# Kernel tuning notes

Hardware: AMD Instinct MI355X
Metric: run time of the kernel (lower is better)

## Reference

```python
import jax, jax.numpy as jnp
import numpy as np

N_ATOMS = 16384
APC = 64            # atoms per conformer
N_CONF = 256        # 64 mols * 4 confs
N_MOL = 64
DEG = 32
E = N_ATOMS * DEG
H = 128             # hidden_channels = num_filters = out_channels
G = 50              # num_gaussians
L = 6               # num_interactions
CUTOFF = 10.0
LOG2 = float(np.log(2.0))


def ssp(x):
    # ShiftedSoftplus: softplus(x) - log(2)
    return jax.nn.softplus(x) - LOG2


def setup_inputs() -> dict:
    key = jax.random.key(0)
    ks = jax.random.split(key, 24)
    rng = np.random.default_rng(0)

    z = jnp.asarray(rng.integers(1, 100, size=(N_ATOMS,)), dtype=jnp.int64 if jax.config.jax_enable_x64 else jnp.int32)
    # positions uniform in a 5A box -> all intra-conformer distances < cutoff
    pos = jax.random.uniform(ks[0], (N_ATOMS, 3), dtype=jnp.float32) * 5.0

    # within-conformer random edges, no self loops (radius_graph surrogate)
    i = np.repeat(np.arange(N_ATOMS), DEG)
    off = rng.integers(1, APC, size=E)
    j = (i // APC) * APC + (i % APC + off) % APC
    edge_index = jnp.asarray(np.stack([j, i]), dtype=jnp.int32)  # [2,E] (source, target)

    atom_to_conf = jnp.asarray(np.arange(N_ATOMS) // APC, dtype=jnp.int32)
    conf_to_mol = jnp.asarray(np.arange(N_CONF) // (N_CONF // N_MOL), dtype=jnp.int32)

    s = 0.05
    p = {
        'emb':     jax.random.normal(ks[1], (120, H), jnp.float32) * s,
        # per-interaction stacked params [L, ...]
        'mlp_w1':  jax.random.normal(ks[2], (L, G, H), jnp.float32) * s,
        'mlp_b1':  jnp.zeros((L, H), jnp.float32),
        'mlp_w2':  jax.random.normal(ks[3], (L, H, H), jnp.float32) * s,
        'mlp_b2':  jnp.zeros((L, H), jnp.float32),
        'cf_w1':   jax.random.normal(ks[4], (L, H, H), jnp.float32) * s,
        'cf_w2':   jax.random.normal(ks[5], (L, H, H), jnp.float32) * s,
        'cf_b2':   jnp.zeros((L, H), jnp.float32),
        'int_w':   jax.random.normal(ks[6], (L, H, H), jnp.float32) * s,
        'int_b':   jnp.zeros((L, H), jnp.float32),
        # readout head
        'out_w1':  jax.random.normal(ks[7], (H, H), jnp.float32) * s,
        'out_b1':  jnp.zeros((H,), jnp.float32),
        'out_w2':  jax.random.normal(ks[8], (H, H), jnp.float32) * s,
        'out_b2':  jnp.zeros((H,), jnp.float32),
        'head_w1': jax.random.normal(ks[9], (H, H // 2), jnp.float32) * s,
        'head_b1': jnp.zeros((H // 2,), jnp.float32),
        'head_w2': jax.random.normal(ks[10], (H // 2, 1), jnp.float32) * s,
        'head_b2': jnp.zeros((1,), jnp.float32),
    }
    return dict(z=z, pos=pos, edge_index=edge_index, atom_to_conf=atom_to_conf,
                conf_to_mol=conf_to_mol, **p)


def reference(z, pos, edge_index, atom_to_conf, conf_to_mol, emb,
              mlp_w1, mlp_b1, mlp_w2, mlp_b2, cf_w1, cf_w2, cf_b2,
              int_w, int_b, out_w1, out_b1, out_w2, out_b2,
              head_w1, head_b1, head_w2, head_b2):
    row, col = edge_index[0], edge_index[1]  # message from row, aggregated at col

    h = emb[z]                                             # [N,H]
    edge_weight = jnp.linalg.norm(pos[row] - pos[col], axis=-1)  # [E]

    # GaussianSmearing
    offset = jnp.linspace(0.0, CUTOFF, G)
    coeff = -0.5 / (offset[1] - offset[0]) ** 2
    edge_attr = jnp.exp(coeff * (edge_weight[:, None] - offset[None, :]) ** 2)  # [E,G]

    C = 0.5 * (jnp.cos(edge_weight * jnp.pi / CUTOFF) + 1.0)  # cosine cutoff [E]

    for l in range(L):
        # filter network on edge features, modulated by cutoff envelope
        Wf = ssp(edge_attr @ mlp_w1[l] + mlp_b1[l]) @ mlp_w2[l] + mlp_b2[l]
        Wf = Wf * C[:, None]                               # [E,H]
        xf = h @ cf_w1[l]                                  # lin1 (no bias) [N,H]
        msg = xf[row] * Wf                                 # gather * filter [E,H]
        agg = jax.ops.segment_sum(msg, col, num_segments=N_ATOMS)  # scatter-add [N,H]
        xc = agg @ cf_w2[l] + cf_b2[l]                     # lin2
        h = h + (ssp(xc) @ int_w[l] + int_b[l])            # act, lin, residual

    h = ssp(h @ out_w1 + out_b1)
    h = h @ out_w2 + out_b2                                # [N,H]

    conf_emb = jax.ops.segment_sum(h, atom_to_conf, num_segments=N_CONF)   # [C,H]
    mol_emb = jax.ops.segment_sum(conf_emb, conf_to_mol, num_segments=N_MOL)  # [M,H]

    out = (ssp(mol_emb @ head_w1 + head_b1) @ head_w2 + head_b2)[:, 0]  # [M]
    return out
```

## Files before the change

### kernel.cpp

```cpp
#include <hip/hip_runtime.h>
#include <math.h>

#define N_ATOMS 16384
#define APC 64
#define N_CONF 256
#define N_MOL 64
#define DEG 32
#define NEDGE (N_ATOMS * DEG)
#define H 128
#define G 50
#define NL 6
#define TP0 512
#define TPB 4096
#define CUTOFF 10.0f

typedef __attribute__((ext_vector_type(8))) short short8_t;
typedef __attribute__((ext_vector_type(4))) float f32x4;

__device__ __forceinline__ float ssp_f(float x) {
  float e = __expf(-fabsf(x));
  return fmaxf(x, 0.f) + __logf(1.f + e) - 0.69314718055994531f;
}
__device__ __forceinline__ unsigned short bf16_rne(float x) {
  unsigned u = __float_as_uint(x);
  unsigned r = u + 0x7FFF + ((u >> 16) & 1);
  return (unsigned short)(r >> 16);
}
__device__ __forceinline__ float bf16_to_f(unsigned short s) {
  return __uint_as_float(((unsigned)s) << 16);
}
__device__ __forceinline__ float bflo(unsigned u) { return __uint_as_float(u << 16); }
__device__ __forceinline__ float bfhi(unsigned u) { return __uint_as_float(u & 0xFFFF0000u); }

__global__ __launch_bounds__(256) void k_setup(
    const float* __restrict__ cf_w1, const float* __restrict__ cf_w2,
    const float* __restrict__ int_w, const float* __restrict__ out_w1,
    const float* __restrict__ out_w2, short* __restrict__ PW,
    const float* __restrict__ w1, const float* __restrict__ b1,
    const float* __restrict__ w2, const float* __restrict__ b2,
    float* __restrict__ T) {
  __shared__ float g2[2][64];
  __shared__ float S2[2][128];
  const int b = blockIdx.x;
  const int tid = threadIdx.x;
  if (b < 160) {
    int e = b * 256 + tid;
    int g = e >> 11, t = e & 2047;
    int kb = t >> 9, rem = t & 511, nt = rem >> 6, lane = rem & 63;
    int quad = lane >> 4, ln = lane & 15;
    int kbase = kb * 32 + quad * 8;
    int n = nt * 16 + ln;
    const float* src;
    if (g < 12) {
      int l = g >> 1;
      src = (g & 1) ? (int_w + l * 16384) : (cf_w2 + l * 16384);
    } else if (g < 18) {
      src = cf_w1 + (g - 12) * 16384;
    } else {
      src = (g == 18) ? out_w1 : out_w2;
    }
    short hv[8], lv[8];
    #pragma unroll
    for (int j = 0; j < 8; j++) {
      float x = src[(kbase + j) * H + n];
      unsigned short hb = bf16_rne(x);
      hv[j] = (short)hb;
      lv[j] = (short)bf16_rne(x - bf16_to_f(hb));
    }
    size_t base = (size_t)g * 32768 + (size_t)t * 8;
    *(short8_t*)&PW[base] = *(short8_t*)hv;
    *(short8_t*)&PW[base + 16384] = *(short8_t*)lv;
  } else {
    int bb = b - 160;
    const int l = bb >> 8;
    const int grp = tid >> 7;
    const int c = tid & 127;
    const int p = (bb & 255) * 2 + grp;
    const float d = (float)p * (CUTOFF / (float)(TP0 - 1));
    const float gspace = CUTOFF / (float)(G - 1);
    const float coeff = -0.5f / (gspace * gspace);
    if (c < G) {
      float x = d - (float)c * gspace;
      g2[grp][c] = __expf(coeff * x * x);
    }
    __syncthreads();
    const float* W1 = w1 + l * G * H;
    float s = b1[l * H + c];
    #pragma unroll 5
    for (int i = 0; i < G; i++) s += g2[grp][i] * W1[i * H + c];
    S2[grp][c] = ssp_f(s);
    __syncthreads();
    const float* W2 = w2 + l * H * H;
    float o = b2[l * H + c];
    #pragma unroll 8
    for (int j = 0; j < H; j++) o += S2[grp][j] * W2[j * H + c];
    float Cc = 0.5f * (__cosf(d * (3.14159265358979f / CUTOFF)) + 1.f);
    T[((size_t)l * TP0 + p) * H + c] = o * Cc;
  }
}

__global__ __launch_bounds__(256) void k_up(const float* __restrict__ T,
                                            unsigned short* __restrict__ Tb) {
  int t = blockIdx.x * 256 + threadIdx.x;
  int l = t >> 17;
  int rem = t & 131071;
  int p4 = rem >> 5, cg = rem & 31;
  int c = cg * 4;
  float u = (float)p4 * ((float)(TP0 - 1) / (float)(TPB - 1));
  int i = (int)u;
  if (i > TP0 - 2) i = TP0 - 2;
  float f = u - (float)i;
  const float* a = T + ((size_t)l * TP0 + i) * H + c;
  float4 v0 = *(const float4*)a;
  float4 v1 = *(const float4*)(a + H);
  ushort4 o;
  o.x = bf16_rne(v0.x + f * (v1.x - v0.x));
  o.y = bf16_rne(v0.y + f * (v1.y - v0.y));
  o.z = bf16_rne(v0.z + f * (v1.z - v0.z));
  o.w = bf16_rne(v0.w + f * (v1.w - v0.w));
  *(ushort4*)&Tb[((size_t)l * TPB + p4) * H + c] = o;
}

#define MFMA(a, b, c) __builtin_amdgcn_mfma_f32_16x16x32_bf16((a), (b), (c), 0, 0, 0)

__device__ __forceinline__ void load_afrags(const short (*AH)[136], const short (*AL)[136],
                                            int rt, int ln, int quad,
                                            short8_t ah[4], short8_t al[4]) {
  #pragma unroll
  for (int kb = 0; kb < 4; kb++) {
    int ko = kb * 32 + quad * 8;
    ah[kb] = *(const short8_t*)&AH[rt * 16 + ln][ko];
    al[kb] = *(const short8_t*)&AL[rt * 16 + ln][ko];
  }
}

__device__ __forceinline__ void gemm2w(const short8_t ah[4], const short8_t al[4],
                                       const short* __restrict__ pw, int nt0, int lane,
                                       f32x4 acc[2]) {
  #pragma unroll
  for (int ct = 0; ct < 2; ct++) {
    int nt = nt0 + ct;
    f32x4 a = {0.f, 0.f, 0.f, 0.f};
    #pragma unroll
    for (int kb = 0; kb < 4; kb++) {
      const short* pb = pw + ((size_t)(kb * 8 + nt) * 64 + lane) * 8;
      short8_t bh = *(const short8_t*)pb;
      short8_t bl = *(const short8_t*)(pb + 16384);
      a = MFMA(ah[kb], bh, a);
      a = MFMA(ah[kb], bl, a);
      a = MFMA(al[kb], bh, a);
    }
    acc[ct] = a;
  }
}

__global__ __launch_bounds__(1024, 1) void k_mega(
    const int* __restrict__ z, const float* __restrict__ pos,
    const int* __restrict__ esrc, const float* __restrict__ emb,
    const unsigned short* __restrict__ Tb, const short* __restrict__ PW,
    const float* __restrict__ cf_b2, const float* __restrict__ int_b,
    const float* __restrict__ out_b1, const float* __restrict__ out_b2,
    float* __restrict__ ce, const float* __restrict__ hw1,
    const float* __restrict__ hb1, const float* __restrict__ hw2,
    const float* __restrict__ hb2, int* __restrict__ cnt,
    float* __restrict__ outp) {
  __shared__ float xs[64][132];
  __shared__ __align__(16) short hH[64][136], hL[64][136];
  __shared__ __align__(16) short S1H[64][136], S1L[64][136];
  __shared__ int pks[2048];
  __shared__ float ps[4][128];
  __shared__ float posL[192];
  __shared__ int is_last;
  const int conf = blockIdx.x;
  const int tid = threadIdx.x;
  const int lane = tid & 63, w = tid >> 6;
  const int quad = lane >> 4, ln = lane & 15;
  const int rt = w & 3, nt0 = (w >> 2) * 2;
  const int eg = lane >> 4, ch0 = (lane & 15) * 8;

  if (tid < 192) posL[tid] = pos[conf * 192 + tid];
  __syncthreads();
  #pragma unroll
  for (int k = 0; k < 2; k++) {
    int e2 = k * 1024 + tid;
    int r = esrc[conf * 2048 + e2];
    int rl = r & (APC - 1);
    int ca = e2 >> 5;
    float dx = posL[rl * 3 + 0] - posL[ca * 3 + 0];
    float dy = posL[rl * 3 + 1] - posL[ca * 3 + 1];
    float dz = posL[rl * 3 + 2] - posL[ca * 3 + 2];
    float d = sqrtf(dx * dx + dy * dy + dz * dz);
    int i = (int)(d * ((float)(TPB - 1) / CUTOFF) + 0.5f);
    if (i > TPB - 1) i = TPB - 1;
    if (i < 0) i = 0;
    pks[e2] = i | (rl << 16);
  }
  {
    int r = tid >> 4, cb = (tid & 15) * 8;
    const float* src = emb + (size_t)z[conf * 64 + r] * H + cb;
    float4 v0 = *(const float4*)src, v1 = *(const float4*)(src + 4);
    float vv[8] = {v0.x, v0.y, v0.z, v0.w, v1.x, v1.y, v1.z, v1.w};
    short hv[8], lv[8];
    #pragma unroll
    for (int u = 0; u < 8; u++) {
      unsigned short hb = bf16_rne(vv[u]);
      hv[u] = (short)hb;
      lv[u] = (short)bf16_rne(vv[u] - bf16_to_f(hb));
    }
    *(short8_t*)&hH[r][cb] = *(short8_t*)hv;
    *(short8_t*)&hL[r][cb] = *(short8_t*)lv;
  }
  __syncthreads();

  {
    short8_t ah[4], al_[4];
    load_afrags(hH, hL, rt, ln, quad, ah, al_);
    f32x4 acc[2];
    gemm2w(ah, al_, PW + (size_t)12 * 32768, nt0, lane, acc);
    #pragma unroll
    for (int ct = 0; ct < 2; ct++)
      #pragma unroll
      for (int reg = 0; reg < 4; reg++)
        xs[rt * 16 + quad * 4 + reg][(nt0 + ct) * 16 + ln] = acc[ct][reg];
  }
  __syncthreads();

  for (int l = 0; l < NL; l++) {
    const unsigned short* Tl = Tb + (size_t)l * TPB * H;
    #pragma unroll 1
    for (int aa = 0; aa < 4; aa++) {
      int a2 = w * 4 + aa;
      int ms[8];
      uint4 tvv[8];
      #pragma unroll
      for (int it = 0; it < 8; it++) ms[it] = pks[a2 * DEG + it * 4 + eg];
      #pragma unroll
      for (int it = 0; it < 8; it++)
        tvv[it] = *(const uint4*)&Tl[(size_t)(ms[it] & 0xFFFF) * H + ch0];
      float acc[8] = {};
      #pragma unroll
      for (int it = 0; it < 8; it++) {
        int sl = ms[it] >> 16;
        const float* xr = &xs[sl][ch0];
        float4 x0 = *(const float4*)xr;
        float4 x1 = *(const float4*)(xr + 4);
        uint4 tv = tvv[it];
        acc[0] += bflo(tv.x) * x0.x; acc[1] += bfhi(tv.x) * x0.y;
        acc[2] += bflo(tv.y) * x0.z; acc[3] += bfhi(tv.y) * x0.w;
        acc[4] += bflo(tv.z) * x1.x; acc[5] += bfhi(tv.z) * x1.y;
        acc[6] += bflo(tv.w) * x1.z; acc[7] += bfhi(tv.w) * x1.w;
      }
      #pragma unroll
      for (int j = 0; j < 8; j++) {
        acc[j] += __shfl_xor(acc[j], 16);
        acc[j] += __shfl_xor(acc[j], 32);
      }
      if (eg == 0) {
        short hv[8], lv[8];
        #pragma unroll
        for (int j = 0; j < 8; j++) {
          unsigned short hb = bf16_rne(acc[j]);
          hv[j] = (short)hb;
          lv[j] = (short)bf16_rne(acc[j] - bf16_to_f(hb));
        }
        *(short8_t*)&S1H[a2][ch0] = *(short8_t*)hv;
        *(short8_t*)&S1L[a2][ch0] = *(short8_t*)lv;
      }
    }
    __syncthreads();
    {
      short8_t ah[4], al_[4];
      load_afrags(S1H, S1L, rt, ln, quad, ah, al_);
      f32x4 acc[2];
      gemm2w(ah, al_, PW + (size_t)(2 * l) * 32768, nt0, lane, acc);
      __syncthreads();
      #pragma unroll
      for (int ct = 0; ct < 2; ct++) {
        int col = (nt0 + ct) * 16 + ln;
        float bb = cf_b2[l * H + col];
        #pragma unroll
        for (int reg = 0; reg < 4; reg++) {
          int row = rt * 16 + quad * 4 + reg;
          float v = ssp_f(acc[ct][reg] + bb);
          unsigned short hb = bf16_rne(v);
          S1H[row][col] = (short)hb;
          S1L[row][col] = (short)bf16_rne(v - bf16_to_f(hb));
        }
      }
    }
    __syncthreads();
    {
      short8_t ah[4], al_[4];
      load_afrags(S1H, S1L, rt, ln, quad, ah, al_);
      f32x4 acc[2];
      gemm2w(ah, al_, PW + (size_t)(2 * l + 1) * 32768, nt0, lane, acc);
      #pragma unroll
      for (int ct = 0; ct < 2; ct++) {
        int col = (nt0 + ct) * 16 + ln;
        float bb = int_b[l * H + col];
        #pragma unroll
        for (int reg = 0; reg < 4; reg++) {
          int row = rt * 16 + quad * 4 + reg;
          float hv = bf16_to_f((unsigned short)hH[row][col]) +
                     bf16_to_f((unsigned short)hL[row][col]);
          float v = acc[ct][reg] + bb + hv;
          unsigned short hb = bf16_rne(v);
          hH[row][col] = (short)hb;
          hL[row][col] = (short)bf16_rne(v - bf16_to_f(hb));
        }
      }
    }
    __syncthreads();
    if (l < NL - 1) {
      short8_t ah[4], al_[4];
      load_afrags(hH, hL, rt, ln, quad, ah, al_);
      f32x4 acc[2];
      gemm2w(ah, al_, PW + (size_t)(13 + l) * 32768, nt0, lane, acc);
      #pragma unroll
      for (int ct = 0; ct < 2; ct++)
        #pragma unroll
        for (int reg = 0; reg < 4; reg++)
          xs[rt * 16 + quad * 4 + reg][(nt0 + ct) * 16 + ln] = acc[ct][reg];
      __syncthreads();
    }
  }

  {
    short8_t ah[4], al_[4];
    load_afrags(hH, hL, rt, ln, quad, ah, al_);
    f32x4 acc[2];
    gemm2w(ah, al_, PW + (size_t)18 * 32768, nt0, lane, acc);
    __syncthreads();
    #pragma unroll
    for (int ct = 0; ct < 2; ct++) {
      int col = (nt0 + ct) * 16 + ln;
      float bb = out_b1[col];
      #pragma unroll
      for (int reg = 0; reg < 4; reg++) {
        int row = rt * 16 + quad * 4 + reg;
        float v = ssp_f(acc[ct][reg] + bb);
        unsigned short hb = bf16_rne(v);
        S1H[row][col] = (short)hb;
        S1L[row][col] = (short)bf16_rne(v - bf16_to_f(hb));
      }
    }
  }
  __syncthreads();
  {
    short8_t ah[4], al_[4];
    load_afrags(S1H, S1L, rt, ln, quad, ah, al_);
    f32x4 acc[2];
    gemm2w(ah, al_, PW + (size_t)19 * 32768, nt0, lane, acc);
    #pragma unroll
    for (int ct = 0; ct < 2; ct++) {
      int col = (nt0 + ct) * 16 + ln;
      float s = acc[ct][0] + acc[ct][1] + acc[ct][2] + acc[ct][3];
      s += __shfl_xor(s, 16);
      s += __shfl_xor(s, 32);
      if (quad == 0) ps[rt][col] = s;
    }
  }
  __syncthreads();
  if (tid < 128) {
    float v = ps[0][tid] + ps[1][tid] + ps[2][tid] + ps[3][tid] + 64.f * out_b2[tid];
    __hip_atomic_store(&ce[conf * 128 + tid], v, __ATOMIC_RELAXED,
                       __HIP_MEMORY_SCOPE_AGENT);
  }
  __syncthreads();
  if (tid == 0) {
    __threadfence();
    int old = __hip_atomic_fetch_add(cnt, 1, __ATOMIC_ACQ_REL,
                                     __HIP_MEMORY_SCOPE_AGENT);
    is_last = (old == N_CONF - 1) ? 1 : 0;
  }
  __syncthreads();
  if (is_last) {
    __threadfence();
    float* mol = &xs[0][0];
    for (int t = tid; t < N_MOL * 128; t += 1024) {
      int m = t >> 7, c = t & 127;
      const float* bb = ce + (size_t)(m * 4) * 128;
      float s = __hip_atomic_load(&bb[c], __ATOMIC_RELAXED, __HIP_MEMORY_SCOPE_AGENT) +
                __hip_atomic_load(&bb[128 + c], __ATOMIC_RELAXED, __HIP_MEMORY_SCOPE_AGENT) +
                __hip_atomic_load(&bb[256 + c], __ATOMIC_RELAXED, __HIP_MEMORY_SCOPE_AGENT) +
                __hip_atomic_load(&bb[384 + c], __ATOMIC_RELAXED, __HIP_MEMORY_SCOPE_AGENT);
      mol[t] = s;
    }
    __syncthreads();
    float* q = (float*)&S1H[0][0];
    for (int t = tid; t < N_MOL * 64; t += 1024) {
      int m = t >> 6, j = t & 63;
      float qq = hb1[j];
      #pragma unroll 8
      for (int c = 0; c < H; c++) qq += mol[m * 128 + c] * hw1[c * 64 + j];
      q[t] = ssp_f(qq);
    }
    __syncthreads();
    if (tid < N_MOL) {
      float o = hb2[0];
      #pragma unroll 8
      for (int j = 0; j < 64; j++) o += q[tid * 64 + j] * hw2[j];
      outp[tid] = o;
    }
  }
}

extern "C" void kernel_launch(void* const* d_in, const int* in_sizes, int n_in,
                              void* d_out, int out_size, void* d_ws, size_t ws_size,
                              hipStream_t stream) {
  const int*   z       = (const int*)d_in[0];
  const float* pos     = (const float*)d_in[1];
  const int*   eidx    = (const int*)d_in[2];
  const float* emb     = (const float*)d_in[5];
  const float* mlp_w1  = (const float*)d_in[6];
  const float* mlp_b1  = (const float*)d_in[7];
  const float* mlp_w2  = (const float*)d_in[8];
  const float* mlp_b2  = (const float*)d_in[9];
  const float* cf_w1   = (const float*)d_in[10];
  const float* cf_w2   = (const float*)d_in[11];
  const float* cf_b2   = (const float*)d_in[12];
  const float* int_w   = (const float*)d_in[13];
  const float* int_b   = (const float*)d_in[14];
  const float* out_w1  = (const float*)d_in[15];
  const float* out_b1  = (const float*)d_in[16];
  const float* out_w2  = (const float*)d_in[17];
  const float* out_b2  = (const float*)d_in[18];
  const float* head_w1 = (const float*)d_in[19];
  const float* head_b1 = (const float*)d_in[20];
  const float* head_w2 = (const float*)d_in[21];
  const float* head_b2 = (const float*)d_in[22];

  char* ws = (char*)d_ws;
  float*          T   = (float*)ws;
  unsigned short* Tb  = (unsigned short*)(ws + 1572864);
  short*          PW  = (short*)(ws + 1572864 + 6291456);
  float*          ce  = (float*)(ws + 9175040);
  int*            cnt = (int*)(ws + 9306112);

  hipMemsetAsync(cnt, 0, 4, stream);
  k_setup<<<1696, 256, 0, stream>>>(cf_w1, cf_w2, int_w, out_w1, out_w2, PW,
                                    mlp_w1, mlp_b1, mlp_w2, mlp_b2, T);
  k_up<<<(NL * TPB * H / 4) / 256, 256, 0, stream>>>(T, Tb);
  k_mega<<<N_CONF, 1024, 0, stream>>>(z, pos, eidx, emb, Tb, PW, cf_b2, int_b,
                                      out_b1, out_b2, ce,
                                      head_w1, head_b1, head_w2, head_b2,
                                      cnt, (float*)d_out);
}
```

Baseline: 260.2 us.

## Fuse table upsampling into mega kernel with grid barrier; retile GEMM waves

Removes the separate k_up launch by having every block of k_mega upsample its slice of the bf16 filter table, then wait on a global atomic-counter barrier before the interaction layers read it. The GEMM wave mapping also changes: each wave now computes two 16-row tiles for one 16-column tile, reusing each B fragment across two MFMAs instead of reusing A fragments across two column tiles. The grid barrier relies on all 256 blocks being co-resident, which holds only if the GPU has at least 256 CUs at one block per CU. It also adds spin-wait latency.

```diff
diff --git a/kernel.cpp b/kernel.cpp
--- a/kernel.cpp
+++ b/kernel.cpp
@@ -99,65 +99,35 @@
   }
 }
 
-__global__ __launch_bounds__(256) void k_up(const float* __restrict__ T,
-                                            unsigned short* __restrict__ Tb) {
-  int t = blockIdx.x * 256 + threadIdx.x;
-  int l = t >> 17;
-  int rem = t & 131071;
-  int p4 = rem >> 5, cg = rem & 31;
-  int c = cg * 4;
-  float u = (float)p4 * ((float)(TP0 - 1) / (float)(TPB - 1));
-  int i = (int)u;
-  if (i > TP0 - 2) i = TP0 - 2;
-  float f = u - (float)i;
-  const float* a = T + ((size_t)l * TP0 + i) * H + c;
-  float4 v0 = *(const float4*)a;
-  float4 v1 = *(const float4*)(a + H);
-  ushort4 o;
-  o.x = bf16_rne(v0.x + f * (v1.x - v0.x));
-  o.y = bf16_rne(v0.y + f * (v1.y - v0.y));
-  o.z = bf16_rne(v0.z + f * (v1.z - v0.z));
-  o.w = bf16_rne(v0.w + f * (v1.w - v0.w));
-  *(ushort4*)&Tb[((size_t)l * TPB + p4) * H + c] = o;
-}
-
 #define MFMA(a, b, c) __builtin_amdgcn_mfma_f32_16x16x32_bf16((a), (b), (c), 0, 0, 0)
 
-__device__ __forceinline__ void load_afrags(const short (*AH)[136], const short (*AL)[136],
-                                            int rt, int ln, int quad,
-                                            short8_t ah[4], short8_t al[4]) {
+__device__ __forceinline__ void gemm_rt2(const short (*AH)[136], const short (*AL)[136],
+                                         const short* __restrict__ pw,
+                                         int rt2, int nt, int lane, int quad, int ln,
+                                         f32x4 acc[2]) {
   #pragma unroll
   for (int kb = 0; kb < 4; kb++) {
+    const short* pb = pw + ((size_t)(kb * 8 + nt) * 64 + lane) * 8;
+    short8_t bh = *(const short8_t*)pb;
+    short8_t bl = *(const short8_t*)(pb + 16384);
     int ko = kb * 32 + quad * 8;
-    ah[kb] = *(const short8_t*)&AH[rt * 16 + ln][ko];
-    al[kb] = *(const short8_t*)&AL[rt * 16 + ln][ko];
-  }
-}
-
-__device__ __forceinline__ void gemm2w(const short8_t ah[4], const short8_t al[4],
-                                       const short* __restrict__ pw, int nt0, int lane,
-                                       f32x4 acc[2]) {
-  #pragma unroll
-  for (int ct = 0; ct < 2; ct++) {
-    int nt = nt0 + ct;
-    f32x4 a = {0.f, 0.f, 0.f, 0.f};
-    #pragma unroll
-    for (int kb = 0; kb < 4; kb++) {
-      const short* pb = pw + ((size_t)(kb * 8 + nt) * 64 + lane) * 8;
-      short8_t bh = *(const short8_t*)pb;
-      short8_t bl = *(const short8_t*)(pb + 16384);
-      a = MFMA(ah[kb], bh, a);
-      a = MFMA(ah[kb], bl, a);
-      a = MFMA(al[kb], bh, a);
-    }
-    acc[ct] = a;
+    #pragma unroll
+    for (int rtt = 0; rtt < 2; rtt++) {
+      int row = rt2 * 32 + rtt * 16 + ln;
+      short8_t ah = *(const short8_t*)&AH[row][ko];
+      short8_t al = *(const short8_t*)&AL[row][ko];
+      acc[rtt] = MFMA(ah, bh, acc[rtt]);
+      acc[rtt] = MFMA(ah, bl, acc[rtt]);
+      acc[rtt] = MFMA(al, bh, acc[rtt]);
+    }
   }
 }
 
 __global__ __launch_bounds__(1024, 1) void k_mega(
     const int* __restrict__ z, const float* __restrict__ pos,
     const int* __restrict__ esrc, const float* __restrict__ emb,
-    const unsigned short* __restrict__ Tb, const short* __restrict__ PW,
+    const float* __restrict__ T, unsigned short* __restrict__ Tb,
+    const short* __restrict__ PW,
     const float* __restrict__ cf_b2, const float* __restrict__ int_b,
     const float* __restrict__ out_b1, const float* __restrict__ out_b2,
     float* __restrict__ ce, const float* __restrict__ hw1,
@@ -168,14 +138,14 @@
   __shared__ __align__(16) short hH[64][136], hL[64][136];
   __shared__ __align__(16) short S1H[64][136], S1L[64][136];
   __shared__ int pks[2048];
-  __shared__ float ps[4][128];
+  __shared__ float ps[2][128];
   __shared__ float posL[192];
   __shared__ int is_last;
   const int conf = blockIdx.x;
   const int tid = threadIdx.x;
   const int lane = tid & 63, w = tid >> 6;
   const int quad = lane >> 4, ln = lane & 15;
-  const int rt = w & 3, nt0 = (w >> 2) * 2;
+  const int rt2 = w & 1, nt = w >> 1;
   const int eg = lane >> 4, ch0 = (lane & 15) * 8;
 
   if (tid < 192) posL[tid] = pos[conf * 192 + tid];
@@ -210,20 +180,52 @@
     *(short8_t*)&hH[r][cb] = *(short8_t*)hv;
     *(short8_t*)&hL[r][cb] = *(short8_t*)lv;
   }
-  __syncthreads();
-
   {
-    short8_t ah[4], al_[4];
-    load_afrags(hH, hL, rt, ln, quad, ah, al_);
-    f32x4 acc[2];
-    gemm2w(ah, al_, PW + (size_t)12 * 32768, nt0, lane, acc);
-    #pragma unroll
-    for (int ct = 0; ct < 2; ct++)
+    int gt = conf * 1024 + tid;
+    #pragma unroll
+    for (int k = 0; k < 3; k++) {
+      int t = gt + k * 262144;
+      int l = t >> 17;
+      int rem = t & 131071;
+      int p4 = rem >> 5, cg = rem & 31;
+      int c = cg * 4;
+      float u = (float)p4 * ((float)(TP0 - 1) / (float)(TPB - 1));
+      int i = (int)u;
+      if (i > TP0 - 2) i = TP0 - 2;
+      float f = u - (float)i;
+      const float* a = T + ((size_t)l * TP0 + i) * H + c;
+      float4 v0 = *(const float4*)a;
+      float4 v1 = *(const float4*)(a + H);
+      ushort4 o;
+      o.x = bf16_rne(v0.x + f * (v1.x - v0.x));
+      o.y = bf16_rne(v0.y + f * (v1.y - v0.y));
+      o.z = bf16_rne(v0.z + f * (v1.z - v0.z));
+      o.w = bf16_rne(v0.w + f * (v1.w - v0.w));
+      *(ushort4*)&Tb[((size_t)l * TPB + p4) * H + c] = o;
+    }
+  }
+  __syncthreads();
+
+  {
+    f32x4 acc[2] = {{0.f, 0.f, 0.f, 0.f}, {0.f, 0.f, 0.f, 0.f}};
+    gemm_rt2(hH, hL, PW + (size_t)12 * 32768, rt2, nt, lane, quad, ln, acc);
+    int col = nt * 16 + ln;
+    #pragma unroll
+    for (int rtt = 0; rtt < 2; rtt++)
       #pragma unroll
       for (int reg = 0; reg < 4; reg++)
-        xs[rt * 16 + quad * 4 + reg][(nt0 + ct) * 16 + ln] = acc[ct][reg];
-  }
-  __syncthreads();
+        xs[rt2 * 32 + rtt * 16 + quad * 4 + reg][col] = acc[rtt][reg];
+  }
+  __threadfence();
+  __syncthreads();
+  if (tid == 0) {
+    __hip_atomic_fetch_add(&cnt[0], 1, __ATOMIC_ACQ_REL, __HIP_MEMORY_SCOPE_AGENT);
+    while (__hip_atomic_load(&cnt[0], __ATOMIC_ACQUIRE, __HIP_MEMORY_SCOPE_AGENT)
+           != N_CONF)
+      __builtin_amdgcn_s_sleep(32);
+  }
+  __syncthreads();
+  __threadfence();
 
   for (int l = 0; l < NL; l++) {
     const unsigned short* Tl = Tb + (size_t)l * TPB * H;
@@ -269,107 +271,93 @@
     }
     __syncthreads();
     {
-      short8_t ah[4], al_[4];
-      load_afrags(S1H, S1L, rt, ln, quad, ah, al_);
-      f32x4 acc[2];
-      gemm2w(ah, al_, PW + (size_t)(2 * l) * 32768, nt0, lane, acc);
+      f32x4 acc[2] = {{0.f, 0.f, 0.f, 0.f}, {0.f, 0.f, 0.f, 0.f}};
+      gemm_rt2(S1H, S1L, PW + (size_t)(2 * l) * 32768, rt2, nt, lane, quad, ln, acc);
       __syncthreads();
-      #pragma unroll
-      for (int ct = 0; ct < 2; ct++) {
-        int col = (nt0 + ct) * 16 + ln;
-        float bb = cf_b2[l * H + col];
+      int col = nt * 16 + ln;
+      float bb = cf_b2[l * H + col];
+      #pragma unroll
+      for (int rtt = 0; rtt < 2; rtt++)
         #pragma unroll
         for (int reg = 0; reg < 4; reg++) {
-          int row = rt * 16 + quad * 4 + reg;
-          float v = ssp_f(acc[ct][reg] + bb);
+          int row = rt2 * 32 + rtt * 16 + quad * 4 + reg;
+          float v = ssp_f(acc[rtt][reg] + bb);
           unsigned short hb = bf16_rne(v);
           S1H[row][col] = (short)hb;
           S1L[row][col] = (short)bf16_rne(v - bf16_to_f(hb));
         }
-      }
     }
     __syncthreads();
     {
-      short8_t ah[4], al_[4];
-      load_afrags(S1H, S1L, rt, ln, quad, ah, al_);
-      f32x4 acc[2];
-      gemm2w(ah, al_, PW + (size_t)(2 * l + 1) * 32768, nt0, lane, acc);
-      #pragma unroll
-      for (int ct = 0; ct < 2; ct++) {
-        int col = (nt0 + ct) * 16 + ln;
-        float bb = int_b[l * H + col];
+      f32x4 acc[2] = {{0.f, 0.f, 0.f, 0.f}, {0.f, 0.f, 0.f, 0.f}};
+      gemm_rt2(S1H, S1L, PW + (size_t)(2 * l + 1) * 32768, rt2, nt, lane, quad, ln, acc);
+      int col = nt * 16 + ln;
+      float bb = int_b[l * H + col];
+      #pragma unroll
+      for (int rtt = 0; rtt < 2; rtt++)
         #pragma unroll
         for (int reg = 0; reg < 4; reg++) {
-          int row = rt * 16 + quad * 4 + reg;
+          int row = rt2 * 32 + rtt * 16 + quad * 4 + reg;
           float hv = bf16_to_f((unsigned short)hH[row][col]) +
                      bf16_to_f((unsigned short)hL[row][col]);
-          float v = acc[ct][reg] + bb + hv;
+          float v = acc[rtt][reg] + bb + hv;
           unsigned short hb = bf16_rne(v);
           hH[row][col] = (short)hb;
           hL[row][col] = (short)bf16_rne(v - bf16_to_f(hb));
         }
-      }
     }
     __syncthreads();
     if (l < NL - 1) {
-      short8_t ah[4], al_[4];
-      load_afrags(hH, hL, rt, ln, quad, ah, al_);
-      f32x4 acc[2];
-      gemm2w(ah, al_, PW + (size_t)(13 + l) * 32768, nt0, lane, acc);
-      #pragma unroll
-      for (int ct = 0; ct < 2; ct++)
+      f32x4 acc[2] = {{0.f, 0.f, 0.f, 0.f}, {0.f, 0.f, 0.f, 0.f}};
+      gemm_rt2(hH, hL, PW + (size_t)(13 + l) * 32768, rt2, nt, lane, quad, ln, acc);
+      int col = nt * 16 + ln;
+      #pragma unroll
+      for (int rtt = 0; rtt < 2; rtt++)
         #pragma unroll
         for (int reg = 0; reg < 4; reg++)
-          xs[rt * 16 + quad * 4 + reg][(nt0 + ct) * 16 + ln] = acc[ct][reg];
+          xs[rt2 * 32 + rtt * 16 + quad * 4 + reg][col] = acc[rtt][reg];
       __syncthreads();
     }
   }
 
   {
-    short8_t ah[4], al_[4];
-    load_afrags(hH, hL, rt, ln, quad, ah, al_);
-    f32x4 acc[2];
-    gemm2w(ah, al_, PW + (size_t)18 * 32768, nt0, lane, acc);
-    __syncthreads();
-    #pragma unroll
-    for (int ct = 0; ct < 2; ct++) {
-      int col = (nt0 + ct) * 16 + ln;
-      float bb = out_b1[col];
+    f32x4 acc[2] = {{0.f, 0.f, 0.f, 0.f}, {0.f, 0.f, 0.f, 0.f}};
+    gemm_rt2(hH, hL, PW + (size_t)18 * 32768, rt2, nt, lane, quad, ln, acc);
+    __syncthreads();
+    int col = nt * 16 + ln;
+    float bb = out_b1[col];
+    #pragma unroll
+    for (int rtt = 0; rtt < 2; rtt++)
       #pragma unroll
       for (int reg = 0; reg < 4; reg++) {
-        int row = rt * 16 + quad * 4 + reg;
-        float v = ssp_f(acc[ct][reg] + bb);
+        int row = rt2 * 32 + rtt * 16 + quad * 4 + reg;
+        float v = ssp_f(acc[rtt][reg] + bb);
         unsigned short hb = bf16_rne(v);
         S1H[row][col] = (short)hb;
         S1L[row][col] = (short)bf16_rne(v - bf16_to_f(hb));
       }
-    }
   }
   __syncthreads();
   {
-    short8_t ah[4], al_[4];
-    load_afrags(S1H, S1L, rt, ln, quad, ah, al_);
-    f32x4 acc[2];
-    gemm2w(ah, al_, PW + (size_t)19 * 32768, nt0, lane, acc);
-    #pragma unroll
-    for (int ct = 0; ct < 2; ct++) {
-      int col = (nt0 + ct) * 16 + ln;
-      float s = acc[ct][0] + acc[ct][1] + acc[ct][2] + acc[ct][3];
-      s += __shfl_xor(s, 16);
-      s += __shfl_xor(s, 32);
-      if (quad == 0) ps[rt][col] = s;
-    }
+    f32x4 acc[2] = {{0.f, 0.f, 0.f, 0.f}, {0.f, 0.f, 0.f, 0.f}};
+    gemm_rt2(S1H, S1L, PW + (size_t)19 * 32768, rt2, nt, lane, quad, ln, acc);
+    int col = nt * 16 + ln;
+    float s = acc[0][0] + acc[0][1] + acc[0][2] + acc[0][3] +
+              acc[1][0] + acc[1][1] + acc[1][2] + acc[1][3];
+    s += __shfl_xor(s, 16);
+    s += __shfl_xor(s, 32);
+    if (quad == 0) ps[rt2][col] = s;
   }
   __syncthreads();
   if (tid < 128) {
-    float v = ps[0][tid] + ps[1][tid] + ps[2][tid] + ps[3][tid] + 64.f * out_b2[tid];
+    float v = ps[0][tid] + ps[1][tid] + 64.f * out_b2[tid];
     __hip_atomic_store(&ce[conf * 128 + tid], v, __ATOMIC_RELAXED,
                        __HIP_MEMORY_SCOPE_AGENT);
   }
   __syncthreads();
   if (tid == 0) {
     __threadfence();
-    int old = __hip_atomic_fetch_add(cnt, 1, __ATOMIC_ACQ_REL,
+    int old = __hip_atomic_fetch_add(&cnt[1], 1, __ATOMIC_ACQ_REL,
                                      __HIP_MEMORY_SCOPE_AGENT);
     is_last = (old == N_CONF - 1) ? 1 : 0;
   }
@@ -437,11 +425,10 @@
   float*          ce  = (float*)(ws + 9175040);
   int*            cnt = (int*)(ws + 9306112);
 
-  hipMemsetAsync(cnt, 0, 4, stream);
+  hipMemsetAsync(cnt, 0, 8, stream);
   k_setup<<<1696, 256, 0, stream>>>(cf_w1, cf_w2, int_w, out_w1, out_w2, PW,
                                     mlp_w1, mlp_b1, mlp_w2, mlp_b2, T);
-  k_up<<<(NL * TPB * H / 4) / 256, 256, 0, stream>>>(T, Tb);
-  k_mega<<<N_CONF, 1024, 0, stream>>>(z, pos, eidx, emb, Tb, PW, cf_b2, int_b,
+  k_mega<<<N_CONF, 1024, 0, stream>>>(z, pos, eidx, emb, T, Tb, PW, cf_b2, int_b,
                                       out_b1, out_b2, ce,
                                       head_w1, head_b1, head_w2, head_b2,
                                       cnt, (float*)d_out);
```

Measured after the change: 369.1 us. +41.9%, slower.
